# Performance work log

Hardware: AMD Instinct MI355X
Metric: run time of the kernel (lower is better)

Reference implementation:

```python
import jax, jax.numpy as jnp
import numpy as np
from jax import lax

# Solver hyper-params for the smoothed robust-OT LP (fixed-iteration, jit-safe)
N_STEPS = 60
TAU = 0.05    # softmax temperature smoothing max over classes
RHO = 10.0    # quadratic penalty weight on the Wasserstein-cost constraint
LR = 0.5


def setup_inputs() -> dict:
    key = jax.random.key(0)
    ks = jax.random.split(key, 6)
    X = jax.random.normal(ks[0], (16, 96, 3, 64, 64), jnp.float32)
    Qr = jax.random.uniform(ks[1], (16, 10, 96), jnp.float32) + 0.1
    Q = Qr / Qr.sum(-1, keepdims=True)  # each (b,k) row is a distribution over samples
    conv_w = jax.random.normal(ks[2], (32, 3, 3, 3), jnp.float32) * 0.05
    conv_b = jnp.zeros((32,), jnp.float32)
    fc_w = jax.random.normal(ks[3], (256, 30752), jnp.float32) * 0.01
    fc_b = jnp.zeros((256,), jnp.float32)
    theta = jnp.ones((10,), jnp.float32) * 0.1
    return {"X": X, "Q": Q, "conv_w": conv_w, "conv_b": conv_b,
            "fc_w": fc_w, "fc_b": fc_b, "theta": theta}


def _features(X, conv_w, conv_b, fc_w, fc_b):
    B, S = X.shape[:2]
    x = X.reshape(B * S, *X.shape[2:])  # [B*S, C, H, W]
    x = lax.conv_general_dilated(x, conv_w, window_strides=(1, 1), padding='VALID',
                                 dimension_numbers=('NCHW', 'OIHW', 'NCHW'))
    x = jax.nn.relu(x + conv_b[None, :, None, None])
    x = lax.reduce_window(x, -jnp.inf, lax.max, (1, 1, 2, 2), (1, 1, 2, 2), 'VALID')
    # dropout is identity in eval mode
    x = x.reshape(B * S, -1)
    x = jax.nn.relu(x @ fc_w.T + fc_b)
    return x.reshape(B, S, -1)  # [B, S, F]


def _pairwise_sqdist(feats):
    n2 = (feats ** 2).sum(-1)  # [B, S]
    D = n2[:, :, None] + n2[:, None, :] - 2.0 * jnp.einsum('bif,bjf->bij', feats, feats)
    diag = jnp.diagonal(D, axis1=1, axis2=2)  # [B, S]
    return jnp.clip(D - diag[:, None, :], 0.0)


def _robust_ot_solve(D, Q, theta):
    # Approximate the CvxpyLayer LP:
    #   min_gamma sum_l max_k p_k[l]  s.t. gamma_k rows sum to Q_k, <gamma_k, C> <= theta_k
    # via mirror-descent on a row-stochastic parameterization (rows of gamma_k are
    # Q_k[i]-scaled softmaxes), with a smoothed max (logsumexp) and quadratic penalty.
    B, K, S = Q.shape

    def obj(A):
        gamma = Q[..., None] * jax.nn.softmax(A, axis=-1)      # [B,K,S,S]
        p = gamma.sum(axis=2)                                   # column sums [B,K,S]
        smooth_max = TAU * jax.nn.logsumexp(p / TAU, axis=1)    # [B,S]
        cost = jnp.einsum('bkij,bij->bk', gamma, D)             # [B,K]
        pen = jnp.sum(jax.nn.relu(cost - theta[None, :]) ** 2)
        return smooth_max.sum() + RHO * pen

    grad_obj = jax.grad(obj)

    @jax.checkpoint
    def step(A, _):
        return A - LR * grad_obj(A), None

    A0 = jnp.zeros((B, K, S, S), D.dtype)
    A, _ = lax.scan(step, A0, None, length=N_STEPS)
    gamma = Q[..., None] * jax.nn.softmax(A, axis=-1)
    return gamma.sum(axis=2)  # p_hat [B,K,S]


def reference(X, Q, conv_w, conv_b, fc_w, fc_b, theta):
    feats = _features(X, conv_w, conv_b, fc_w, fc_b)   # [B,S,F]
    D = _pairwise_sqdist(feats)                        # [B,S,S]
    p_hat = _robust_ot_solve(D, Q, theta)              # [B,K,S]
    return p_hat
```

## Files before the change

### kernel.cpp

```cpp
#include <hip/hip_runtime.h>

#define BB 16
#define SS 96
#define KK 10
#define FF 256
#define IH 64
#define IW 64
#define OCH 32
#define PH 31
#define PW 31
#define NPOS 961
#define FDIM 30752
#define NIMG 1536

#define TAUI 20.0f
#define RHOC 10.0f
#define LRC  0.5f
#define NSTEPS 60

#define KSPLIT 31
#define KCHE 992

typedef _Float16 v8hf __attribute__((ext_vector_type(8)));
typedef _Float16 v4hf __attribute__((ext_vector_type(4)));
typedef __fp16 h2 __attribute__((ext_vector_type(2)));
typedef float v4f __attribute__((ext_vector_type(4)));

__global__ __launch_bounds__(256)
void wcast(const float* __restrict__ w, _Float16* __restrict__ wh) {
    const size_t i = ((size_t)blockIdx.x * 256 + threadIdx.x) * 4;
    float4 v = *(const float4*)(w + i);
    v4hf o = {(_Float16)v.x, (_Float16)v.y, (_Float16)v.z, (_Float16)v.w};
    *(v4hf*)(wh + i) = o;
}

__global__ __launch_bounds__(64)
void wprep(const float* __restrict__ w, __fp16* __restrict__ wp) {
    const int t = blockIdx.x * 64 + threadIdx.x;
    if (t >= 288) return;
    const float* s = w + t * 3;
    const __fp16 w0 = (__fp16)s[0], w1 = (__fp16)s[1], w2 = (__fp16)s[2];
    __fp16* d = wp + t * 8;
    d[0] = w0; d[1] = w1;
    d[2] = w2; d[3] = (__fp16)0.f;
    d[4] = (__fp16)0.f; d[5] = w0;
    d[6] = w1; d[7] = w2;
}

__global__ __launch_bounds__(256)
void conv_pool(const float* __restrict__ X, const uint4* __restrict__ wp,
               const float* __restrict__ bias, _Float16* __restrict__ pooled) {
    __shared__ uint4 wsl[288];
    const int tid = threadIdx.x;
    for (int i = tid; i < 288; i += 256) wsl[i] = wp[i];
    __syncthreads();

    const int img = blockIdx.y;
    const int pos = blockIdx.x * 256 + tid;
    if (pos >= NPOS) return;
    const int oy = pos / PW, ox = pos % PW;
    const int iy = 2 * oy, ix = 2 * ox;
    const float* xb = X + (size_t)img * 3 * IH * IW;
    h2 inh[3][4][2];
#pragma unroll
    for (int c = 0; c < 3; c++)
#pragma unroll
        for (int r = 0; r < 4; r++) {
            const float* row = xb + ((size_t)c * IH + iy + r) * IW + ix;
            float2 p0 = *(const float2*)(row);
            float2 p1 = *(const float2*)(row + 2);
            inh[c][r][0] = __builtin_amdgcn_cvt_pkrtz(p0.x, p0.y);
            inh[c][r][1] = __builtin_amdgcn_cvt_pkrtz(p1.x, p1.y);
        }
    _Float16* outp = pooled + (size_t)img * FDIM + pos;
    for (int oc = 0; oc < OCH; oc++) {
        float a00 = 0.f, a01 = 0.f, a10 = 0.f, a11 = 0.f;
#pragma unroll
        for (int c = 0; c < 3; c++)
#pragma unroll
            for (int ky = 0; ky < 3; ky++) {
                const h2* q = (const h2*)(wsl + oc * 9 + c * 3 + ky);
                a00 = __builtin_amdgcn_fdot2(inh[c][ky][0], q[0], a00, false);
                a00 = __builtin_amdgcn_fdot2(inh[c][ky][1], q[1], a00, false);
                a01 = __builtin_amdgcn_fdot2(inh[c][ky][0], q[2], a01, false);
                a01 = __builtin_amdgcn_fdot2(inh[c][ky][1], q[3], a01, false);
                a10 = __builtin_amdgcn_fdot2(inh[c][ky + 1][0], q[0], a10, false);
                a10 = __builtin_amdgcn_fdot2(inh[c][ky + 1][1], q[1], a10, false);
                a11 = __builtin_amdgcn_fdot2(inh[c][ky + 1][0], q[2], a11, false);
                a11 = __builtin_amdgcn_fdot2(inh[c][ky + 1][1], q[3], a11, false);
            }
        float m = fmaxf(fmaxf(a00, a01), fmaxf(a10, a11)) + bias[oc];
        outp[(size_t)oc * NPOS] = (_Float16)fmaxf(m, 0.f);
    }
}

__global__ __launch_bounds__(256)
void fc_gemm(const _Float16* __restrict__ Ah, const _Float16* __restrict__ Wh,
             float* __restrict__ fpart) {
    __shared__ _Float16 Asl[128 * 56];
    __shared__ _Float16 Bsl[128 * 56];
    const int m0 = blockIdx.x * 128, n0 = blockIdx.y * 128;
    const int k0 = blockIdx.z * KCHE;
    const int tid = threadIdx.x;
    const int wave = tid >> 6, lane = tid & 63;
    const int quad = lane >> 4, l16 = lane & 15;
    const int wm = (wave & 1) * 64, wn = (wave >> 1) * 64;
    const int ar = tid >> 1, ac = (tid & 1) * 16;
    const _Float16* Ag = Ah + (size_t)(m0 + ar) * FDIM + ac;
    const _Float16* Bg = Wh + (size_t)(n0 + ar) * FDIM + ac;

    v4f acc[4][4];
#pragma unroll
    for (int i = 0; i < 4; i++)
#pragma unroll
        for (int j = 0; j < 4; j++) acc[i][j] = (v4f)(0.f);

    for (int s = 0; s < KCHE / 32; s++) {
        const int gk = k0 + (s << 5);
        uint4 a0 = *(const uint4*)(Ag + gk);
        uint4 a1 = *(const uint4*)(Ag + gk + 8);
        uint4 b0 = *(const uint4*)(Bg + gk);
        uint4 b1 = *(const uint4*)(Bg + gk + 8);
        __syncthreads();
        *(uint4*)&Asl[ar * 56 + ac] = a0;
        *(uint4*)&Asl[ar * 56 + ac + 8] = a1;
        *(uint4*)&Bsl[ar * 56 + ac] = b0;
        *(uint4*)&Bsl[ar * 56 + ac + 8] = b1;
        __syncthreads();
        v8hf af[4], bf[4];
#pragma unroll
        for (int mt = 0; mt < 4; mt++)
            af[mt] = *(const v8hf*)&Asl[(wm + mt * 16 + l16) * 56 + quad * 8];
#pragma unroll
        for (int nt = 0; nt < 4; nt++)
            bf[nt] = *(const v8hf*)&Bsl[(wn + nt * 16 + l16) * 56 + quad * 8];
#pragma unroll
        for (int mt = 0; mt < 4; mt++)
#pragma unroll
            for (int nt = 0; nt < 4; nt++)
                acc[mt][nt] = __builtin_amdgcn_mfma_f32_16x16x32_f16(
                    af[mt], bf[nt], acc[mt][nt], 0, 0, 0);
    }
    float* outz = fpart + (size_t)blockIdx.z * NIMG * FF;
#pragma unroll
    for (int mt = 0; mt < 4; mt++)
#pragma unroll
        for (int nt = 0; nt < 4; nt++)
#pragma unroll
            for (int i = 0; i < 4; i++) {
                const int gm = m0 + wm + mt * 16 + quad * 4 + i;
                const int gn = n0 + wn + nt * 16 + l16;
                outz[(size_t)gm * FF + gn] = acc[mt][nt][i];
            }
}

__global__ __launch_bounds__(256)
void bias_sum_relu(const float* __restrict__ fpart, const float* __restrict__ bias,
                   float* __restrict__ f) {
    const size_t idx = ((size_t)blockIdx.x * 256 + threadIdx.x) * 4;
    float4 s = make_float4(0.f, 0.f, 0.f, 0.f);
#pragma unroll
    for (int z = 0; z < KSPLIT; z++) {
        float4 v = *(const float4*)(fpart + (size_t)z * NIMG * FF + idx);
        s.x += v.x; s.y += v.y; s.z += v.z; s.w += v.w;
    }
    const int col = (int)(idx & (FF - 1));
    float4 bv = *(const float4*)(bias + col);
    float4 o;
    o.x = fmaxf(s.x + bv.x, 0.f);
    o.y = fmaxf(s.y + bv.y, 0.f);
    o.z = fmaxf(s.z + bv.z, 0.f);
    o.w = fmaxf(s.w + bv.w, 0.f);
    *(float4*)(f + idx) = o;
}

__global__ __launch_bounds__(512)
void rownorm(const float* __restrict__ feats, float* __restrict__ n2) {
    const int b = blockIdx.x;
    const int tid = threadIdx.x, hw = tid >> 5, l = tid & 31;
#pragma unroll
    for (int r = 0; r < 6; r++) {
        const int row = hw * 6 + r;
        const float* fr = feats + ((size_t)b * SS + row) * FF;
        float s = 0.f;
#pragma unroll
        for (int u = 0; u < 8; u++) { float v = fr[l + 32 * u]; s += v * v; }
#pragma unroll
        for (int mm = 16; mm >= 1; mm >>= 1) s += __shfl_xor(s, mm);
        if (l == 0) n2[b * SS + row] = s;
    }
}

__global__ __launch_bounds__(256)
void dmat(const float* __restrict__ feats, const float* __restrict__ n2,
          float* __restrict__ Dm) {
    const int i0 = blockIdx.x * 16, j0 = blockIdx.y * 16, b = blockIdx.z;
    __shared__ float fi[16][260], fj[16][260];
    const int tid = threadIdx.x;
    const int r = tid >> 4, c0 = (tid & 15) * 16;
    const float* fbase = feats + (size_t)b * SS * FF;
#pragma unroll
    for (int v = 0; v < 16; v += 4) {
        float4 a = *(const float4*)(fbase + (size_t)(i0 + r) * FF + c0 + v);
        float4 w = *(const float4*)(fbase + (size_t)(j0 + r) * FF + c0 + v);
        *(float4*)&fi[r][c0 + v] = a;
        *(float4*)&fj[r][c0 + v] = w;
    }
    __syncthreads();
    const int ti = tid >> 4, tj = tid & 15;
    float dot = 0.f;
#pragma unroll 4
    for (int f = 0; f < FF; f += 4) {
        float4 a = *(const float4*)&fi[ti][f];
        float4 w = *(const float4*)&fj[tj][f];
        dot += a.x * w.x + a.y * w.y + a.z * w.z + a.w * w.w;
    }
    const int i = i0 + ti, j = j0 + tj;
    const float d = n2[b * SS + i] + n2[b * SS + j] - 2.f * dot;
    Dm[((size_t)b * SS + i) * SS + j] = fmaxf(d, 0.f);
}

__global__ __launch_bounds__(512)
void ot_kernel(const float* __restrict__ Dg, const float* __restrict__ Qg,
               const float* __restrict__ thetag, float* __restrict__ ppub,
               unsigned* __restrict__ bar, float* __restrict__ out) {
    const int bk = blockIdx.x;
    const int b = bk / KK, k = bk % KK;
    const int tid = threadIdx.x;
    const int hw = tid >> 5, l = tid & 31;

    __shared__ float ppart[16][SS];
    __shared__ float cpart[16];
    __shared__ float Msh[SS];
    __shared__ float pown[SS];
    __shared__ float costsh, lamsh;

    float a[6][3], e[6][3], dre[6][3], rz[6], qi[6];

    const float* Db = Dg + (size_t)b * SS * SS;
    const float* Qb = Qg + ((size_t)b * KK + k) * SS;
#pragma unroll
    for (int r = 0; r < 6; r++) {
        const int i = hw * 6 + r;
#pragma unroll
        for (int u = 0; u < 3; u++) dre[r][u] = Db[i * SS + l + 32 * u];
        qi[r] = Qb[i];
    }
    const float th = thetag[k];
    unsigned* ctr = bar + b * 64;
    unsigned target = 0;

    auto publish_and_wait = [&](int buf) {
        if (tid < SS)
            __hip_atomic_store(&ppub[(((size_t)buf * BB + b) * KK + k) * SS + tid],
                               pown[tid], __ATOMIC_RELAXED, __HIP_MEMORY_SCOPE_AGENT);
        asm volatile("s_waitcnt vmcnt(0)" ::: "memory");
        __syncthreads();
        target += KK;
        if (tid == 0) {
            __hip_atomic_fetch_add(ctr, 1u, __ATOMIC_RELAXED, __HIP_MEMORY_SCOPE_AGENT);
            while (__hip_atomic_load(ctr, __ATOMIC_RELAXED, __HIP_MEMORY_SCOPE_AGENT) < target)
                __builtin_amdgcn_s_sleep(2);
        }
        __syncthreads();
    };

    auto collect = [&]() {
        __syncthreads();
        if (tid < SS) {
            float s = 0.f;
#pragma unroll
            for (int h = 0; h < 16; h++) s += ppart[h][tid];
            pown[tid] = s;
        }
        if (tid == 0) {
            float c = 0.f;
#pragma unroll
            for (int h = 0; h < 16; h++) c += cpart[h];
            costsh = c;
            lamsh = 2.f * RHOC * fmaxf(c - th, 0.f);
        }
        __syncthreads();
    };

    {
        float cd[6];
#pragma unroll
        for (int r = 0; r < 6; r++) {
#pragma unroll
            for (int u = 0; u < 3; u++) { a[r][u] = 0.f; e[r][u] = 1.f; }
            rz[r] = 1.f / 96.f;
            cd[r] = dre[r][0] + dre[r][1] + dre[r][2];
        }
#pragma unroll
        for (int mm = 16; mm >= 1; mm >>= 1)
#pragma unroll
            for (int r = 0; r < 6; r++) cd[r] += __shfl_xor(cd[r], mm);
        float pp0 = 0.f, cc = 0.f;
#pragma unroll
        for (int r = 0; r < 6; r++) {
            const float scale = qi[r] * rz[r];
            pp0 += scale;
            cc += scale * cd[r];
        }
        ppart[hw][l] = pp0; ppart[hw][l + 32] = pp0; ppart[hw][l + 64] = pp0;
        if (l == 0) cpart[hw] = cc;
        collect();
    }
    publish_and_wait(0);

    for (int t = 0; t < NSTEPS; t++) {
        const int rbuf = t & 1;
        if (tid < SS) {
            const float* ps = ppub + (((size_t)rbuf * BB + b) * KK) * SS + tid;
            float v[KK];
            float mx = -1e30f;
#pragma unroll
            for (int kk2 = 0; kk2 < KK; kk2++) {
                v[kk2] = __hip_atomic_load(&ps[kk2 * SS], __ATOMIC_RELAXED,
                                           __HIP_MEMORY_SCOPE_AGENT) * TAUI;
                mx = fmaxf(mx, v[kk2]);
            }
            float sum = 0.f;
#pragma unroll
            for (int kk2 = 0; kk2 < KK; kk2++) sum += __expf(v[kk2] - mx);
            Msh[tid] = __expf(v[k] - mx) * __builtin_amdgcn_rcpf(sum);
        }
        __syncthreads();
        const float lam = lamsh;
        const float M0 = Msh[l], M1 = Msh[l + 32], M2 = Msh[l + 64];

        float g[6][3], dt[6];
#pragma unroll
        for (int r = 0; r < 6; r++) {
            g[r][0] = fmaf(lam, dre[r][0], M0);
            g[r][1] = fmaf(lam, dre[r][1], M1);
            g[r][2] = fmaf(lam, dre[r][2], M2);
            dt[r] = (e[r][0] * g[r][0] + e[r][1] * g[r][1] + e[r][2] * g[r][2]) * rz[r];
        }
#pragma unroll
        for (int mm = 16; mm >= 1; mm >>= 1)
#pragma unroll
            for (int r = 0; r < 6; r++) dt[r] += __shfl_xor(dt[r], mm);

        float mrow[6];
#pragma unroll
        for (int r = 0; r < 6; r++) {
            const float cq = LRC * qi[r] * rz[r];
            a[r][0] -= cq * e[r][0] * (g[r][0] - dt[r]);
            a[r][1] -= cq * e[r][1] * (g[r][1] - dt[r]);
            a[r][2] -= cq * e[r][2] * (g[r][2] - dt[r]);
            mrow[r] = fmaxf(a[r][0], fmaxf(a[r][1], a[r][2]));
        }
#pragma unroll
        for (int mm = 16; mm >= 1; mm >>= 1)
#pragma unroll
            for (int r = 0; r < 6; r++) mrow[r] = fmaxf(mrow[r], __shfl_xor(mrow[r], mm));

        float zz[6], cd[6];
#pragma unroll
        for (int r = 0; r < 6; r++) {
            e[r][0] = __expf(a[r][0] - mrow[r]);
            e[r][1] = __expf(a[r][1] - mrow[r]);
            e[r][2] = __expf(a[r][2] - mrow[r]);
            zz[r] = e[r][0] + e[r][1] + e[r][2];
            cd[r] = e[r][0] * dre[r][0] + e[r][1] * dre[r][1] + e[r][2] * dre[r][2];
        }
#pragma unroll
        for (int mm = 16; mm >= 1; mm >>= 1)
#pragma unroll
            for (int r = 0; r < 6; r++) {
                zz[r] += __shfl_xor(zz[r], mm);
                cd[r] += __shfl_xor(cd[r], mm);
            }

        float pp0 = 0.f, pp1 = 0.f, pp2 = 0.f, cc = 0.f;
#pragma unroll
        for (int r = 0; r < 6; r++) {
            const float rzz = __builtin_amdgcn_rcpf(zz[r]);
            rz[r] = rzz;
            const float scale = qi[r] * rzz;
            pp0 += scale * e[r][0];
            pp1 += scale * e[r][1];
            pp2 += scale * e[r][2];
            cc += scale * cd[r];
        }
        ppart[hw][l] = pp0; ppart[hw][l + 32] = pp1; ppart[hw][l + 64] = pp2;
        if (l == 0) cpart[hw] = cc;
        collect();
        if (t < NSTEPS - 1) publish_and_wait((t + 1) & 1);
    }
    if (tid < SS) out[((size_t)b * KK + k) * SS + tid] = pown[tid];
}

extern "C" void kernel_launch(void* const* d_in, const int* in_sizes, int n_in,
                              void* d_out, int out_size, void* d_ws, size_t ws_size,
                              hipStream_t stream) {
    const float* X     = (const float*)d_in[0];
    const float* Q     = (const float*)d_in[1];
    const float* convw = (const float*)d_in[2];
    const float* convb = (const float*)d_in[3];
    const float* fcw   = (const float*)d_in[4];
    const float* fcb   = (const float*)d_in[5];
    const float* theta = (const float*)d_in[6];
    float* out = (float*)d_out;

    char* ws = (char*)d_ws;
    size_t off = 0;
    auto take = [&](size_t nbytes) {
        char* p = ws + off;
        off += (nbytes + 255) & ~(size_t)255;
        return (void*)p;
    };
    _Float16* pooled = (_Float16*)take((size_t)NIMG * FDIM * 2);
    _Float16* Wh     = (_Float16*)take((size_t)FF * FDIM * 2);
    float*    fpart  = (float*)take((size_t)KSPLIT * NIMG * FF * 4);
    float*    feats  = (float*)take((size_t)NIMG * FF * 4);
    float*    n2     = (float*)take((size_t)NIMG * 4);
    float*    Dm     = (float*)take((size_t)BB * SS * SS * 4);
    float*    ppub   = (float*)take((size_t)2 * BB * KK * SS * 4);
    __fp16*   wpp    = (__fp16*)take((size_t)288 * 8 * 2);
    unsigned* bar    = (unsigned*)take((size_t)BB * 64 * 4);

    (void)hipMemsetAsync(bar, 0, (size_t)BB * 64 * 4, stream);

    hipLaunchKernelGGL(wcast, dim3((FF * FDIM) / 1024), dim3(256), 0, stream, fcw, Wh);
    hipLaunchKernelGGL(wprep, dim3(5), dim3(64), 0, stream, convw, wpp);
    hipLaunchKernelGGL(conv_pool, dim3(4, NIMG), dim3(256), 0, stream,
                       X, (const uint4*)wpp, convb, pooled);
    hipLaunchKernelGGL(fc_gemm, dim3(12, 2, KSPLIT), dim3(256), 0, stream, pooled, Wh, fpart);
    hipLaunchKernelGGL(bias_sum_relu, dim3(NIMG * FF / 1024), dim3(256), 0, stream, fpart, fcb, feats);
    hipLaunchKernelGGL(rownorm, dim3(BB), dim3(512), 0, stream, feats, n2);
    hipLaunchKernelGGL(dmat, dim3(6, 6, BB), dim3(256), 0, stream, feats, n2, Dm);
    hipLaunchKernelGGL(ot_kernel, dim3(BB * KK), dim3(512), 0, stream, Dm, Q, theta, ppub, bar, out);
}
```

Measured before the change: 608.2 us.

## Replace counter barrier with sequence-tagged 64-bit publishes in OT kernel

Removes the per-batch atomic counter barrier between the ten class blocks. Each block now publishes its column sums as 64-bit words that pack the value with a step sequence number. Readers poll each peer's slot until the tag matches the current step. This drops the fetch-add, the thread-0 spin and two block-wide syncs per step, so threads wait only for the data they need. In exchange each publish is twice as wide, up to 96 threads per block poll instead of one, and the double buffer relies on tags to prevent overwrite races.

```diff
diff --git a/kernel.cpp b/kernel.cpp
--- a/kernel.cpp
+++ b/kernel.cpp
@@ -25,6 +25,12 @@
 typedef _Float16 v4hf __attribute__((ext_vector_type(4)));
 typedef __fp16 h2 __attribute__((ext_vector_type(2)));
 typedef float v4f __attribute__((ext_vector_type(4)));
+typedef unsigned long long u64;
+
+union PU {
+    u64 u;
+    struct { float v; unsigned s; } p;
+};
 
 __global__ __launch_bounds__(256)
 void wcast(const float* __restrict__ w, _Float16* __restrict__ wh) {
@@ -222,8 +228,8 @@
 
 __global__ __launch_bounds__(512)
 void ot_kernel(const float* __restrict__ Dg, const float* __restrict__ Qg,
-               const float* __restrict__ thetag, float* __restrict__ ppub,
-               unsigned* __restrict__ bar, float* __restrict__ out) {
+               const float* __restrict__ thetag, u64* __restrict__ ppub,
+               float* __restrict__ out) {
     const int bk = blockIdx.x;
     const int b = bk / KK, k = bk % KK;
     const int tid = threadIdx.x;
@@ -247,31 +253,18 @@
         qi[r] = Qb[i];
     }
     const float th = thetag[k];
-    unsigned* ctr = bar + b * 64;
-    unsigned target = 0;
-
-    auto publish_and_wait = [&](int buf) {
-        if (tid < SS)
-            __hip_atomic_store(&ppub[(((size_t)buf * BB + b) * KK + k) * SS + tid],
-                               pown[tid], __ATOMIC_RELAXED, __HIP_MEMORY_SCOPE_AGENT);
-        asm volatile("s_waitcnt vmcnt(0)" ::: "memory");
-        __syncthreads();
-        target += KK;
-        if (tid == 0) {
-            __hip_atomic_fetch_add(ctr, 1u, __ATOMIC_RELAXED, __HIP_MEMORY_SCOPE_AGENT);
-            while (__hip_atomic_load(ctr, __ATOMIC_RELAXED, __HIP_MEMORY_SCOPE_AGENT) < target)
-                __builtin_amdgcn_s_sleep(2);
-        }
-        __syncthreads();
-    };
-
-    auto collect = [&]() {
+
+    auto collect_publish = [&](unsigned seq) {
         __syncthreads();
         if (tid < SS) {
             float s = 0.f;
 #pragma unroll
             for (int h = 0; h < 16; h++) s += ppart[h][tid];
             pown[tid] = s;
+            PU w; w.p.v = s; w.p.s = seq;
+            __hip_atomic_store(
+                &ppub[(((size_t)((seq - 1) & 1) * BB + b) * KK + k) * SS + tid],
+                w.u, __ATOMIC_RELAXED, __HIP_MEMORY_SCOPE_AGENT);
         }
         if (tid == 0) {
             float c = 0.f;
@@ -305,22 +298,31 @@
         }
         ppart[hw][l] = pp0; ppart[hw][l + 32] = pp0; ppart[hw][l + 64] = pp0;
         if (l == 0) cpart[hw] = cc;
-        collect();
-    }
-    publish_and_wait(0);
+        collect_publish(1);
+    }
 
     for (int t = 0; t < NSTEPS; t++) {
+        const unsigned seq = (unsigned)t + 1;
         const int rbuf = t & 1;
         if (tid < SS) {
-            const float* ps = ppub + (((size_t)rbuf * BB + b) * KK) * SS + tid;
+            const u64* ps = ppub + (((size_t)rbuf * BB + b) * KK) * SS + tid;
             float v[KK];
+            v[k] = pown[tid] * TAUI;
+            unsigned pend = ((1u << KK) - 1) & ~(1u << k);
+            while (pend) {
+#pragma unroll
+                for (int k2 = 0; k2 < KK; k2++) {
+                    if (pend & (1u << k2)) {
+                        PU r;
+                        r.u = __hip_atomic_load(&ps[(size_t)k2 * SS],
+                                                __ATOMIC_RELAXED, __HIP_MEMORY_SCOPE_AGENT);
+                        if (r.p.s == seq) { v[k2] = r.p.v * TAUI; pend &= ~(1u << k2); }
+                    }
+                }
+            }
             float mx = -1e30f;
 #pragma unroll
-            for (int kk2 = 0; kk2 < KK; kk2++) {
-                v[kk2] = __hip_atomic_load(&ps[kk2 * SS], __ATOMIC_RELAXED,
-                                           __HIP_MEMORY_SCOPE_AGENT) * TAUI;
-                mx = fmaxf(mx, v[kk2]);
-            }
+            for (int kk2 = 0; kk2 < KK; kk2++) mx = fmaxf(mx, v[kk2]);
             float sum = 0.f;
 #pragma unroll
             for (int kk2 = 0; kk2 < KK; kk2++) sum += __expf(v[kk2] - mx);
@@ -387,8 +389,7 @@
         }
         ppart[hw][l] = pp0; ppart[hw][l + 32] = pp1; ppart[hw][l + 64] = pp2;
         if (l == 0) cpart[hw] = cc;
-        collect();
-        if (t < NSTEPS - 1) publish_and_wait((t + 1) & 1);
+        collect_publish(seq + 1);
     }
     if (tid < SS) out[((size_t)b * KK + k) * SS + tid] = pown[tid];
 }
@@ -418,11 +419,10 @@
     float*    feats  = (float*)take((size_t)NIMG * FF * 4);
     float*    n2     = (float*)take((size_t)NIMG * 4);
     float*    Dm     = (float*)take((size_t)BB * SS * SS * 4);
-    float*    ppub   = (float*)take((size_t)2 * BB * KK * SS * 4);
+    u64*      ppub   = (u64*)take((size_t)2 * BB * KK * SS * 8);
     __fp16*   wpp    = (__fp16*)take((size_t)288 * 8 * 2);
-    unsigned* bar    = (unsigned*)take((size_t)BB * 64 * 4);
-
-    (void)hipMemsetAsync(bar, 0, (size_t)BB * 64 * 4, stream);
+
+    (void)hipMemsetAsync(ppub, 0, (size_t)2 * BB * KK * SS * 8, stream);
 
     hipLaunchKernelGGL(wcast, dim3((FF * FDIM) / 1024), dim3(256), 0, stream, fcw, Wh);
     hipLaunchKernelGGL(wprep, dim3(5), dim3(64), 0, stream, convw, wpp);
@@ -432,5 +432,5 @@
     hipLaunchKernelGGL(bias_sum_relu, dim3(NIMG * FF / 1024), dim3(256), 0, stream, fpart, fcb, feats);
     hipLaunchKernelGGL(rownorm, dim3(BB), dim3(512), 0, stream, feats, n2);
     hipLaunchKernelGGL(dmat, dim3(6, 6, BB), dim3(256), 0, stream, feats, n2, Dm);
-    hipLaunchKernelGGL(ot_kernel, dim3(BB * KK), dim3(512), 0, stream, Dm, Q, theta, ppub, bar, out);
-}
+    hipLaunchKernelGGL(ot_kernel, dim3(BB * KK), dim3(512), 0, stream, Dm, Q, theta, ppub, out);
+}
```

Result: slower. 679.7 us (+11.7%).
